# Optimization experiments

Measured on AMD Instinct MI355X. Metric: run time of the kernel, lower is better.

## Reference

```python
import jax, jax.numpy as jnp
import numpy as np
import math

D_MODEL, N_HEADS, D_FF = 1024, 16, 4096
D_K = D_MODEL // N_HEADS
B, S = 4, 2048
EPS = 1e-5


def layer_norm(x, gamma, beta):
    mean = jnp.mean(x, axis=-1, keepdims=True)
    var = jnp.mean((x - mean) ** 2, axis=-1, keepdims=True)  # unbiased=False
    return gamma * (x - mean) / jnp.sqrt(var + EPS) + beta


def setup_inputs() -> dict:
    key = jax.random.key(0)
    ks = jax.random.split(key, 7)
    std_attn = math.sqrt(2.0 / (D_MODEL + D_MODEL))
    std_ff1 = math.sqrt(2.0 / (D_MODEL + D_FF))
    std_ff2 = math.sqrt(2.0 / (D_FF + D_MODEL))
    return {
        "x": jax.random.normal(ks[0], (B, S, D_MODEL), jnp.float32),
        "W_q": jax.random.normal(ks[1], (D_MODEL, D_MODEL), jnp.float32) * std_attn,
        "W_k": jax.random.normal(ks[2], (D_MODEL, D_MODEL), jnp.float32) * std_attn,
        "W_v": jax.random.normal(ks[3], (D_MODEL, D_MODEL), jnp.float32) * std_attn,
        "W_o": jax.random.normal(ks[4], (D_MODEL, D_MODEL), jnp.float32) * std_attn,
        "W1": jax.random.normal(ks[5], (D_MODEL, D_FF), jnp.float32) * std_ff1,
        "b1": jnp.zeros((D_FF,), jnp.float32),
        "W2": jax.random.normal(ks[6], (D_FF, D_MODEL), jnp.float32) * std_ff2,
        "b2": jnp.zeros((D_MODEL,), jnp.float32),
        "ln1_gamma": jnp.ones((D_MODEL,), jnp.float32),
        "ln1_beta": jnp.zeros((D_MODEL,), jnp.float32),
        "ln2_gamma": jnp.ones((D_MODEL,), jnp.float32),
        "ln2_beta": jnp.zeros((D_MODEL,), jnp.float32),
    }


def reference(x, W_q, W_k, W_v, W_o, W1, b1, W2, b2,
              ln1_gamma, ln1_beta, ln2_gamma, ln2_beta):
    b, s, d = x.shape
    # pre-LN attention block
    ln1 = layer_norm(x, ln1_gamma, ln1_beta)
    q = (ln1 @ W_q).reshape(b, s, N_HEADS, D_K)
    k = (ln1 @ W_k).reshape(b, s, N_HEADS, D_K)
    v = (ln1 @ W_v).reshape(b, s, N_HEADS, D_K)
    scores = jnp.einsum("bqhd,bkhd->bhqk", q, k) / math.sqrt(D_K)
    attn = jax.nn.softmax(scores, axis=-1)
    ctx = jnp.einsum("bhqk,bkhd->bqhd", attn, v).reshape(b, s, d)
    attn_out = ctx @ W_o
    attn_residual = x + attn_out
    # pre-LN FFN block
    ln2 = layer_norm(attn_residual, ln2_gamma, ln2_beta)
    ff = jax.nn.relu(ln2 @ W1 + b1) @ W2 + b2
    return attn_residual + ff
```

## Files before the change

### kernel.cpp

```cpp
#include <hip/hip_runtime.h>
#include <hip/hip_bf16.h>

typedef __attribute__((ext_vector_type(4)))  float  floatx4;
typedef __attribute__((ext_vector_type(16))) float  floatx16;
typedef __attribute__((ext_vector_type(8)))  short  shortx8;
typedef __attribute__((ext_vector_type(4)))  short  shortx4;

__device__ __forceinline__ short f2bf(float f) {
    unsigned u = __float_as_uint(f);
    u += 0x7fffu + ((u >> 16) & 1u);
    return (short)(u >> 16);
}
__device__ __forceinline__ float bf2f(short s) {
    return __uint_as_float(((unsigned)(unsigned short)s) << 16);
}
__device__ __forceinline__ float fast_exp2(float x) {
#if __has_builtin(__builtin_amdgcn_exp2f)
    return __builtin_amdgcn_exp2f(x);
#else
    return exp2f(x);
#endif
}

__device__ __forceinline__ void load_lds16(const void* g, void* l) {
    __builtin_amdgcn_global_load_lds(
        (const __attribute__((address_space(1))) unsigned int*)g,
        (__attribute__((address_space(3))) unsigned int*)l,
        16, 0, 0);
}

__global__ __launch_bounds__(256)
void transpose_w(const float* __restrict__ src, short* __restrict__ dst, int K, int N)
{
    __shared__ __align__(16) float tile[32][33];
    const int n0 = blockIdx.x * 32, k0 = blockIdx.y * 32;
    const int tx = threadIdx.x & 31, ty = threadIdx.x >> 5;
    for (int i = 0; i < 32; i += 8)
        tile[ty + i][tx] = src[(size_t)(k0 + ty + i) * N + n0 + tx];
    __syncthreads();
    for (int i = 0; i < 32; i += 8)
        dst[(size_t)(n0 + ty + i) * K + k0 + tx] = f2bf(tile[tx][ty + i]);
}

__global__ __launch_bounds__(256)
void zero_f32(float* __restrict__ p)
{
    const size_t i = (size_t)blockIdx.x * 256 + threadIdx.x;
    reinterpret_cast<float4*>(p)[i] = make_float4(0.f, 0.f, 0.f, 0.f);
}

__global__ __launch_bounds__(256)
void ln_bf16(const float* __restrict__ x, const float* __restrict__ g,
             const float* __restrict__ be, short* __restrict__ out)
{
    const int row = blockIdx.x;
    const int tid = threadIdx.x;
    const float4 v = reinterpret_cast<const float4*>(x + (size_t)row * 1024)[tid];
    float s  = v.x + v.y + v.z + v.w;
    float ss = v.x * v.x + v.y * v.y + v.z * v.z + v.w * v.w;
    for (int off = 32; off > 0; off >>= 1) {
        s  += __shfl_down(s,  off);
        ss += __shfl_down(ss, off);
    }
    __shared__ float rs[4], rss[4];
    const int wave = tid >> 6, lane = tid & 63;
    if (lane == 0) { rs[wave] = s; rss[wave] = ss; }
    __syncthreads();
    const float S    = rs[0] + rs[1] + rs[2] + rs[3];
    const float SS   = rss[0] + rss[1] + rss[2] + rss[3];
    const float mean = S * (1.0f / 1024.0f);
    const float var  = SS * (1.0f / 1024.0f) - mean * mean;
    const float rstd = rsqrtf(var + 1e-5f);
    const float4 gg = reinterpret_cast<const float4*>(g)[tid];
    const float4 bb = reinterpret_cast<const float4*>(be)[tid];
    shortx4 o;
    o[0] = f2bf(gg.x * ((v.x - mean) * rstd) + bb.x);
    o[1] = f2bf(gg.y * ((v.y - mean) * rstd) + bb.y);
    o[2] = f2bf(gg.z * ((v.z - mean) * rstd) + bb.z);
    o[3] = f2bf(gg.w * ((v.w - mean) * rstd) + bb.w);
    *reinterpret_cast<shortx4*>(out + (size_t)row * 1024 + tid * 4) = o;
}

template <int EPI>
__global__ __launch_bounds__(256, 4)
void gemm_bt(const short* __restrict__ A, const short* __restrict__ Bt,
             short* __restrict__ Cb, float* __restrict__ Cf,
             const float* __restrict__ bias, const float* __restrict__ resid,
             int M, int N, int K, int tilesN, int nsplit)
{
    __shared__ __align__(16) short As[128 * 32];
    __shared__ __align__(16) short Bs[128 * 32];

    int wg = blockIdx.x;
    {
        const int nwg = gridDim.x;
        const int q = nwg >> 3, r = nwg & 7;
        const int xcd = wg & 7, loc = wg >> 3;
        wg = (xcd < r ? xcd * (q + 1) : r * (q + 1) + (xcd - r) * q) + loc;
    }
    const int ntiles = gridDim.x / nsplit;
    const int sp   = wg / ntiles;
    const int tile = wg - sp * ntiles;
    const int tm = tile / tilesN, tn = tile - tm * tilesN;
    const size_t bm = (size_t)tm * 128, bn = (size_t)tn * 128;
    const int Ks   = K / nsplit;
    const int kbeg = sp * Ks;

    const int tid  = threadIdx.x;
    const int wave = tid >> 6;
    const int lane = tid & 63;
    const int quad = lane >> 4;
    const int l16  = lane & 15;
    const int wm = wave >> 1, wn = wave & 1;

    floatx4 acc[4][4];
#pragma unroll
    for (int i = 0; i < 4; i++)
#pragma unroll
        for (int j = 0; j < 4; j++)
            acc[i][j] = (floatx4){0.f, 0.f, 0.f, 0.f};

    const int c0 = wave * 2, c1 = wave * 2 + 1;
    const int rA0 = c0 * 16 + (lane >> 2);
    const int rA1 = c1 * 16 + (lane >> 2);
    const int colOff = ((lane & 3) ^ ((lane >> 3) & 3)) * 8;

    const int g0 = (quad ^ ((l16 >> 1) & 3)) * 8;

    for (int k0 = kbeg; k0 < kbeg + Ks; k0 += 32) {
        load_lds16(A  + (bm + rA0) * (size_t)K + k0 + colOff, &As[c0 * 512]);
        load_lds16(A  + (bm + rA1) * (size_t)K + k0 + colOff, &As[c1 * 512]);
        load_lds16(Bt + (bn + rA0) * (size_t)K + k0 + colOff, &Bs[c0 * 512]);
        load_lds16(Bt + (bn + rA1) * (size_t)K + k0 + colOff, &Bs[c1 * 512]);
        __syncthreads();
        shortx8 af[4], bf[4];
#pragma unroll
        for (int mi = 0; mi < 4; mi++)
            af[mi] = *(const shortx8*)&As[(wm * 64 + mi * 16 + l16) * 32 + g0];
#pragma unroll
        for (int ni = 0; ni < 4; ni++)
            bf[ni] = *(const shortx8*)&Bs[(wn * 64 + ni * 16 + l16) * 32 + g0];
#pragma unroll
        for (int mi = 0; mi < 4; mi++)
#pragma unroll
            for (int ni = 0; ni < 4; ni++)
                acc[mi][ni] = __builtin_amdgcn_mfma_f32_16x16x32_bf16(
                    af[mi], bf[ni], acc[mi][ni], 0, 0, 0);
        __syncthreads();
    }

#pragma unroll
    for (int mi = 0; mi < 4; mi++) {
#pragma unroll
        for (int ni = 0; ni < 4; ni++) {
            const size_t row0 = bm + wm * 64 + mi * 16 + quad * 4;
            const size_t col  = bn + wn * 64 + ni * 16 + l16;
#pragma unroll
            for (int r = 0; r < 4; r++) {
                float v = acc[mi][ni][r];
                const size_t idx = (row0 + r) * (size_t)N + col;
                if (EPI == 0) {
                    Cb[idx] = f2bf(v);
                } else if (EPI == 1) {
                    v += bias[col];
                    Cb[idx] = f2bf(v > 0.f ? v : 0.f);
                } else if (EPI == 2) {
                    Cf[idx] = resid[idx] + v;
                } else if (EPI == 4) {
                    if (sp == 0) v += bias[col];
                    atomicAdd(&Cf[idx], v);
                } else {
                    if (sp == 0) v += resid[idx];
                    atomicAdd(&Cf[idx], v);
                }
            }
        }
    }
}

__global__ __launch_bounds__(256)
void transpose_v(const short* __restrict__ qkv, short* __restrict__ vt)
{
    __shared__ __align__(16) short tile[64][65];
    const int st = blockIdx.x, h = blockIdx.y, b = blockIdx.z;
    const int t = threadIdx.x;
    for (int i = 0; i < 2; i++) {
        const int idx = i * 256 + t;
        const int s = idx >> 3, dg = idx & 7;
        shortx8 val = *(const shortx8*)&qkv[(size_t)(b * 2048 + st * 64 + s) * 3072
                                           + 2048 + h * 64 + dg * 8];
        for (int u = 0; u < 8; u++) tile[s][dg * 8 + u] = val[u];
    }
    __syncthreads();
    const int d = t >> 2, sg = (t & 3) * 16;
    shortx8 lo, hi;
    for (int i = 0; i < 8; i++) {
        lo[i] = tile[sg + i][d];
        hi[i] = tile[sg + 8 + i][d];
    }
    const size_t base = ((size_t)(b * 16 + h) * 64 + d) * 2048 + st * 64 + sg;
    *(shortx8*)&vt[base]     = lo;
    *(shortx8*)&vt[base + 8] = hi;
}

__global__ __launch_bounds__(512, 4)
void attention_kernel(const short* __restrict__ qkv, const short* __restrict__ vt,
                      short* __restrict__ ctx)
{
    const int qt = blockIdx.x, h = blockIdx.y, b = blockIdx.z;
    const int tid  = threadIdx.x;
    const int wave = tid >> 6;
    const int lane = tid & 63;
    const int l32  = lane & 31;
    const int hf   = lane >> 5;

    __shared__ __align__(16) short Ks[64 * 72];
    __shared__ __align__(16) short Vs[64 * 72];
    __shared__ __align__(16) short Ps[8][32 * 72];

    const int q0 = qt * 256 + wave * 32;
    const float qscale = 0.125f * 1.44269504088896f;
    const short* qrow = qkv + (size_t)(b * 2048 + q0 + l32) * 3072 + h * 64;
    shortx8 qf[4];
    for (int dk = 0; dk < 4; dk++) {
        shortx8 raw = *(const shortx8*)&qrow[dk * 16 + hf * 8];
        for (int j = 0; j < 8; j++) raw[j] = f2bf(bf2f(raw[j]) * qscale);
        qf[dk] = raw;
    }

    floatx16 accO[2];
    for (int t = 0; t < 2; t++)
        for (int r = 0; r < 16; r++) accO[t][r] = 0.f;
    float lsum = 0.f;

    const short* kbase = qkv + (size_t)(b * 2048) * 3072 + 1024 + h * 64;
    const short* vbase = vt + ((size_t)(b * 16 + h) * 64) * 2048;
    short* const psw = &Ps[wave][0];
    unsigned* const pswd = (unsigned*)psw;

    const int ss = tid >> 3, sdg = tid & 7;

    for (int kt = 0; kt < 32; ++kt) {
        __syncthreads();
        {
            shortx8 kv = *(const shortx8*)&kbase[(size_t)(kt * 64 + ss) * 3072 + sdg * 8];
            *(shortx8*)&Ks[ss * 72 + sdg * 8] = kv;
            shortx8 vv = *(const shortx8*)&vbase[(size_t)ss * 2048 + kt * 64 + sdg * 8];
            *(shortx8*)&Vs[ss * 72 + sdg * 8] = vv;
        }
        __syncthreads();

        for (int t = 0; t < 2; t++) {
            floatx16 c;
            for (int r = 0; r < 16; r++) c[r] = 0.f;
            for (int dk = 0; dk < 4; dk++) {
                shortx8 kf = *(const shortx8*)&Ks[(t * 32 + l32) * 72 + dk * 16 + hf * 8];
                c = __builtin_amdgcn_mfma_f32_32x32x16_bf16(kf, qf[dk], c, 0, 0, 0);
            }
            for (int R = 0; R < 4; R++) {
                float2 a, bb;
                a.x  = fast_exp2(c[4 * R + 0]);
                a.y  = fast_exp2(c[4 * R + 1]);
                bb.x = fast_exp2(c[4 * R + 2]);
                bb.y = fast_exp2(c[4 * R + 3]);
                lsum += (a.x + a.y) + (bb.x + bb.y);
                union { __hip_bfloat162 h2[2]; uint2 u; } pk;
                pk.h2[0] = __float22bfloat162_rn(a);
                pk.h2[1] = __float22bfloat162_rn(bb);
                *(uint2*)&pswd[l32 * 36 + t * 16 + 4 * R + 2 * hf] = pk.u;
            }
        }
        asm volatile("s_waitcnt lgkmcnt(0)" ::: "memory");

        shortx8 pf[4];
        for (int sk = 0; sk < 4; sk++)
            pf[sk] = *(const shortx8*)&psw[l32 * 72 + sk * 16 + hf * 8];

        for (int t = 0; t < 2; t++) {
            floatx16 c = accO[t];
            for (int sk = 0; sk < 4; sk++) {
                shortx8 vf = *(const shortx8*)&Vs[(t * 32 + l32) * 72 + sk * 16 + hf * 8];
                c = __builtin_amdgcn_mfma_f32_32x32x16_bf16(vf, pf[sk], c, 0, 0, 0);
            }
            accO[t] = c;
        }
    }

    const float lfull = lsum + __shfl_xor(lsum, 32);
    const float inv = 1.0f / lfull;
    const size_t crow = (size_t)(b * 2048 + q0 + l32) * 1024 + h * 64;
    for (int t = 0; t < 2; t++)
        for (int R = 0; R < 4; R++) {
            float2 a, bb;
            a.x  = accO[t][4 * R + 0] * inv;
            a.y  = accO[t][4 * R + 1] * inv;
            bb.x = accO[t][4 * R + 2] * inv;
            bb.y = accO[t][4 * R + 3] * inv;
            union { __hip_bfloat162 h2[2]; uint2 u; } pk;
            pk.h2[0] = __float22bfloat162_rn(a);
            pk.h2[1] = __float22bfloat162_rn(bb);
            *(uint2*)&ctx[crow + t * 32 + 8 * R + 4 * hf] = pk.u;
        }
}

extern "C" void kernel_launch(void* const* d_in, const int* in_sizes, int n_in,
                              void* d_out, int out_size, void* d_ws, size_t ws_size,
                              hipStream_t stream)
{
    const float* x   = (const float*)d_in[0];
    const float* Wq  = (const float*)d_in[1];
    const float* Wk  = (const float*)d_in[2];
    const float* Wv  = (const float*)d_in[3];
    const float* Wo  = (const float*)d_in[4];
    const float* W1  = (const float*)d_in[5];
    const float* b1  = (const float*)d_in[6];
    const float* W2  = (const float*)d_in[7];
    const float* b2  = (const float*)d_in[8];
    const float* g1  = (const float*)d_in[9];
    const float* be1 = (const float*)d_in[10];
    const float* g2  = (const float*)d_in[11];
    const float* be2 = (const float*)d_in[12];
    float* out = (float*)d_out;
    char*  ws  = (char*)d_ws;

    const size_t MiB = 1u << 20;
    short* regA   = (short*)(ws);
    short* qkv    = (short*)(ws + 16 * MiB);
    short* vt     = (short*)(ws + 64 * MiB);
    short* ff1    = qkv;
    short* Wqkv_t = (short*)(ws + 80 * MiB);
    short* Wo_t   = (short*)(ws + 86 * MiB);
    short* W1_t   = (short*)(ws + 88 * MiB);
    short* W2_t   = (short*)(ws + 96 * MiB);

    const dim3 blk(256);

    transpose_w<<<dim3(32, 32),  blk, 0, stream>>>(Wq, Wqkv_t,                  1024, 1024);
    transpose_w<<<dim3(32, 32),  blk, 0, stream>>>(Wk, Wqkv_t + 1024 * 1024,    1024, 1024);
    transpose_w<<<dim3(32, 32),  blk, 0, stream>>>(Wv, Wqkv_t + 2 * 1024 * 1024,1024, 1024);
    transpose_w<<<dim3(32, 32),  blk, 0, stream>>>(Wo, Wo_t,                    1024, 1024);
    transpose_w<<<dim3(128, 32), blk, 0, stream>>>(W1, W1_t,                    1024, 4096);
    transpose_w<<<dim3(32, 128), blk, 0, stream>>>(W2, W2_t,                    4096, 1024);

    ln_bf16<<<8192, blk, 0, stream>>>(x, g1, be1, regA);
    gemm_bt<0><<<dim3(1536), blk, 0, stream>>>(regA, Wqkv_t, qkv, nullptr,
                                               nullptr, nullptr, 8192, 3072, 1024, 24, 1);
    transpose_v<<<dim3(32, 16, 4), blk, 0, stream>>>(qkv, vt);
    attention_kernel<<<dim3(8, 16, 4), dim3(512), 0, stream>>>(qkv, vt, regA);
    zero_f32<<<dim3(8192), blk, 0, stream>>>(out);
    gemm_bt<5><<<dim3(1024), blk, 0, stream>>>(regA, Wo_t, nullptr, out,
                                               nullptr, x, 8192, 1024, 1024, 8, 2);
    ln_bf16<<<8192, blk, 0, stream>>>(out, g2, be2, regA);
    gemm_bt<1><<<dim3(2048), blk, 0, stream>>>(regA, W1_t, ff1, nullptr,
                                               b1, nullptr, 8192, 4096, 1024, 32, 1);
    gemm_bt<4><<<dim3(1024), blk, 0, stream>>>(ff1, W2_t, nullptr, out,
                                               b2, nullptr, 8192, 1024, 4096, 8, 2);
}
```

Baseline: 589.6 us.

## Drop split-K and zero-fill for Wo GEMM; map column slabs per XCD

```diff
diff --git a/kernel.cpp b/kernel.cpp
--- a/kernel.cpp
+++ b/kernel.cpp
@@ -40,13 +40,6 @@
     __syncthreads();
     for (int i = 0; i < 32; i += 8)
         dst[(size_t)(n0 + ty + i) * K + k0 + tx] = f2bf(tile[tx][ty + i]);
-}
-
-__global__ __launch_bounds__(256)
-void zero_f32(float* __restrict__ p)
-{
-    const size_t i = (size_t)blockIdx.x * 256 + threadIdx.x;
-    reinterpret_cast<float4*>(p)[i] = make_float4(0.f, 0.f, 0.f, 0.f);
 }
 
 __global__ __launch_bounds__(256)
@@ -91,17 +84,17 @@
     __shared__ __align__(16) short As[128 * 32];
     __shared__ __align__(16) short Bs[128 * 32];
 
-    int wg = blockIdx.x;
-    {
-        const int nwg = gridDim.x;
-        const int q = nwg >> 3, r = nwg & 7;
-        const int xcd = wg & 7, loc = wg >> 3;
-        wg = (xcd < r ? xcd * (q + 1) : r * (q + 1) + (xcd - r) * q) + loc;
-    }
+    const int wg   = blockIdx.x;
+    const int xcd  = wg & 7;
+    const int loc  = wg >> 3;
+    const int cpx  = tilesN >> 3;
     const int ntiles = gridDim.x / nsplit;
-    const int sp   = wg / ntiles;
-    const int tile = wg - sp * ntiles;
-    const int tm = tile / tilesN, tn = tile - tm * tilesN;
+    const int rows  = ntiles / tilesN;
+    const int persp = rows * cpx;
+    const int sp   = loc / persp;
+    const int r    = loc - sp * persp;
+    const int tm   = r / cpx;
+    const int tn   = xcd * cpx + (r - (r / cpx) * cpx);
     const size_t bm = (size_t)tm * 128, bn = (size_t)tn * 128;
     const int Ks   = K / nsplit;
     const int kbeg = sp * Ks;
@@ -156,9 +149,9 @@
             const size_t row0 = bm + wm * 64 + mi * 16 + quad * 4;
             const size_t col  = bn + wn * 64 + ni * 16 + l16;
 #pragma unroll
-            for (int r = 0; r < 4; r++) {
-                float v = acc[mi][ni][r];
-                const size_t idx = (row0 + r) * (size_t)N + col;
+            for (int r2 = 0; r2 < 4; r2++) {
+                float v = acc[mi][ni][r2];
+                const size_t idx = (row0 + r2) * (size_t)N + col;
                 if (EPI == 0) {
                     Cb[idx] = f2bf(v);
                 } else if (EPI == 1) {
@@ -166,11 +159,8 @@
                     Cb[idx] = f2bf(v > 0.f ? v : 0.f);
                 } else if (EPI == 2) {
                     Cf[idx] = resid[idx] + v;
-                } else if (EPI == 4) {
+                } else {
                     if (sp == 0) v += bias[col];
-                    atomicAdd(&Cf[idx], v);
-                } else {
-                    if (sp == 0) v += resid[idx];
                     atomicAdd(&Cf[idx], v);
                 }
             }
@@ -347,9 +337,8 @@
                                                nullptr, nullptr, 8192, 3072, 1024, 24, 1);
     transpose_v<<<dim3(32, 16, 4), blk, 0, stream>>>(qkv, vt);
     attention_kernel<<<dim3(8, 16, 4), dim3(512), 0, stream>>>(qkv, vt, regA);
-    zero_f32<<<dim3(8192), blk, 0, stream>>>(out);
-    gemm_bt<5><<<dim3(1024), blk, 0, stream>>>(regA, Wo_t, nullptr, out,
-                                               nullptr, x, 8192, 1024, 1024, 8, 2);
+    gemm_bt<2><<<dim3(512), blk, 0, stream>>>(regA, Wo_t, nullptr, out,
+                                              nullptr, x, 8192, 1024, 1024, 8, 1);
     ln_bf16<<<8192, blk, 0, stream>>>(out, g2, be2, regA);
     gemm_bt<1><<<dim3(2048), blk, 0, stream>>>(regA, W1_t, ff1, nullptr,
                                                b1, nullptr, 8192, 4096, 1024, 32, 1);
```

Measured after the change: 570.4 us. 3.3% less time.

## Double GEMM K-tile to 64 and drop split-K for the Wo projection

Applied to the files above, without the earlier changes.

```diff
diff --git a/kernel.cpp b/kernel.cpp
--- a/kernel.cpp
+++ b/kernel.cpp
@@ -40,13 +40,6 @@
     __syncthreads();
     for (int i = 0; i < 32; i += 8)
         dst[(size_t)(n0 + ty + i) * K + k0 + tx] = f2bf(tile[tx][ty + i]);
-}
-
-__global__ __launch_bounds__(256)
-void zero_f32(float* __restrict__ p)
-{
-    const size_t i = (size_t)blockIdx.x * 256 + threadIdx.x;
-    reinterpret_cast<float4*>(p)[i] = make_float4(0.f, 0.f, 0.f, 0.f);
 }
 
 __global__ __launch_bounds__(256)
@@ -88,8 +81,8 @@
              const float* __restrict__ bias, const float* __restrict__ resid,
              int M, int N, int K, int tilesN, int nsplit)
 {
-    __shared__ __align__(16) short As[128 * 32];
-    __shared__ __align__(16) short Bs[128 * 32];
+    __shared__ __align__(16) short As[128 * 64];
+    __shared__ __align__(16) short Bs[128 * 64];
 
     int wg = blockIdx.x;
     {
@@ -120,32 +113,54 @@
         for (int j = 0; j < 4; j++)
             acc[i][j] = (floatx4){0.f, 0.f, 0.f, 0.f};
 
-    const int c0 = wave * 2, c1 = wave * 2 + 1;
-    const int rA0 = c0 * 16 + (lane >> 2);
-    const int rA1 = c1 * 16 + (lane >> 2);
-    const int colOff = ((lane & 3) ^ ((lane >> 3) & 3)) * 8;
-
-    const int g0 = (quad ^ ((l16 >> 1) & 3)) * 8;
-
-    for (int k0 = kbeg; k0 < kbeg + Ks; k0 += 32) {
-        load_lds16(A  + (bm + rA0) * (size_t)K + k0 + colOff, &As[c0 * 512]);
-        load_lds16(A  + (bm + rA1) * (size_t)K + k0 + colOff, &As[c1 * 512]);
-        load_lds16(Bt + (bn + rA0) * (size_t)K + k0 + colOff, &Bs[c0 * 512]);
-        load_lds16(Bt + (bn + rA1) * (size_t)K + k0 + colOff, &Bs[c1 * 512]);
+    const int srow = tid >> 3;
+    const int gsrc = (tid & 7) ^ (srow & 7);
+    const short* sA = A  + (bm + srow) * (size_t)K + kbeg + gsrc * 8;
+    const short* sB = Bt + (bn + srow) * (size_t)K + kbeg + gsrc * 8;
+    const int dstw = wave * 512;
+
+    const int g0 = ((quad    ) ^ (l16 & 7)) * 8;
+    const int g1 = ((quad + 4) ^ (l16 & 7)) * 8;
+
+    for (int k0 = 0; k0 < Ks; k0 += 64) {
+#pragma unroll
+        for (int c = 0; c < 4; ++c)
+            load_lds16(sA + (size_t)(c * 32) * K + k0, &As[c * 2048 + dstw]);
+#pragma unroll
+        for (int c = 0; c < 4; ++c)
+            load_lds16(sB + (size_t)(c * 32) * K + k0, &Bs[c * 2048 + dstw]);
         __syncthreads();
-        shortx8 af[4], bf[4];
-#pragma unroll
-        for (int mi = 0; mi < 4; mi++)
-            af[mi] = *(const shortx8*)&As[(wm * 64 + mi * 16 + l16) * 32 + g0];
-#pragma unroll
-        for (int ni = 0; ni < 4; ni++)
-            bf[ni] = *(const shortx8*)&Bs[(wn * 64 + ni * 16 + l16) * 32 + g0];
-#pragma unroll
-        for (int mi = 0; mi < 4; mi++)
+
+        {
+            shortx8 af[4], bf[4];
+#pragma unroll
+            for (int mi = 0; mi < 4; mi++)
+                af[mi] = *(const shortx8*)&As[(wm * 64 + mi * 16 + l16) * 64 + g0];
 #pragma unroll
             for (int ni = 0; ni < 4; ni++)
-                acc[mi][ni] = __builtin_amdgcn_mfma_f32_16x16x32_bf16(
-                    af[mi], bf[ni], acc[mi][ni], 0, 0, 0);
+                bf[ni] = *(const shortx8*)&Bs[(wn * 64 + ni * 16 + l16) * 64 + g0];
+#pragma unroll
+            for (int mi = 0; mi < 4; mi++)
+#pragma unroll
+                for (int ni = 0; ni < 4; ni++)
+                    acc[mi][ni] = __builtin_amdgcn_mfma_f32_16x16x32_bf16(
+                        af[mi], bf[ni], acc[mi][ni], 0, 0, 0);
+        }
+        {
+            shortx8 af[4], bf[4];
+#pragma unroll
+            for (int mi = 0; mi < 4; mi++)
+                af[mi] = *(const shortx8*)&As[(wm * 64 + mi * 16 + l16) * 64 + g1];
+#pragma unroll
+            for (int ni = 0; ni < 4; ni++)
+                bf[ni] = *(const shortx8*)&Bs[(wn * 64 + ni * 16 + l16) * 64 + g1];
+#pragma unroll
+            for (int mi = 0; mi < 4; mi++)
+#pragma unroll
+                for (int ni = 0; ni < 4; ni++)
+                    acc[mi][ni] = __builtin_amdgcn_mfma_f32_16x16x32_bf16(
+                        af[mi], bf[ni], acc[mi][ni], 0, 0, 0);
+        }
         __syncthreads();
     }
 
@@ -156,9 +171,9 @@
             const size_t row0 = bm + wm * 64 + mi * 16 + quad * 4;
             const size_t col  = bn + wn * 64 + ni * 16 + l16;
 #pragma unroll
-            for (int r = 0; r < 4; r++) {
-                float v = acc[mi][ni][r];
-                const size_t idx = (row0 + r) * (size_t)N + col;
+            for (int r2 = 0; r2 < 4; r2++) {
+                float v = acc[mi][ni][r2];
+                const size_t idx = (row0 + r2) * (size_t)N + col;
                 if (EPI == 0) {
                     Cb[idx] = f2bf(v);
                 } else if (EPI == 1) {
@@ -166,11 +181,8 @@
                     Cb[idx] = f2bf(v > 0.f ? v : 0.f);
                 } else if (EPI == 2) {
                     Cf[idx] = resid[idx] + v;
-                } else if (EPI == 4) {
+                } else {
                     if (sp == 0) v += bias[col];
-                    atomicAdd(&Cf[idx], v);
-                } else {
-                    if (sp == 0) v += resid[idx];
                     atomicAdd(&Cf[idx], v);
                 }
             }
@@ -347,9 +359,8 @@
                                                nullptr, nullptr, 8192, 3072, 1024, 24, 1);
     transpose_v<<<dim3(32, 16, 4), blk, 0, stream>>>(qkv, vt);
     attention_kernel<<<dim3(8, 16, 4), dim3(512), 0, stream>>>(qkv, vt, regA);
-    zero_f32<<<dim3(8192), blk, 0, stream>>>(out);
-    gemm_bt<5><<<dim3(1024), blk, 0, stream>>>(regA, Wo_t, nullptr, out,
-                                               nullptr, x, 8192, 1024, 1024, 8, 2);
+    gemm_bt<2><<<dim3(512), blk, 0, stream>>>(regA, Wo_t, nullptr, out,
+                                              nullptr, x, 8192, 1024, 1024, 8, 1);
     ln_bf16<<<8192, blk, 0, stream>>>(out, g2, be2, regA);
     gemm_bt<1><<<dim3(2048), blk, 0, stream>>>(regA, W1_t, ff1, nullptr,
                                                b1, nullptr, 8192, 4096, 1024, 32, 1);
```

New measurement: 528.9 us. 1.11x faster.
